# Optimization experiments

Hardware: AMD Instinct MI355X
Metric: run time of the kernel (lower is better)

The kernel has to match this reference:

```python
import jax, jax.numpy as jnp
import numpy as np

N_NODES = 50000
N_EDGES = 800000
IN_DIM = 96
NUM_HEADS = 8
HEAD_DIM = IN_DIM // NUM_HEADS  # 12


def setup_inputs() -> dict:
    key = jax.random.key(0)
    ks = jax.random.split(key, 11)
    s = 1.0 / np.sqrt(IN_DIM)
    return {
        "x": jax.random.normal(ks[0], (N_NODES, IN_DIM), dtype=jnp.float32),
        "edge_index": jax.random.randint(ks[1], (2, N_EDGES), 0, N_NODES, dtype=jnp.int64),
        "edge_attr": jax.random.normal(ks[2], (N_EDGES, IN_DIM), dtype=jnp.float32),
        # Linear weights stored as [in, out] (apply as x @ W + b)
        "Wq": jax.random.normal(ks[3], (IN_DIM, IN_DIM), dtype=jnp.float32) * s,
        "bq": jax.random.normal(ks[4], (IN_DIM,), dtype=jnp.float32) * s,
        "Wk": jax.random.normal(ks[5], (IN_DIM, IN_DIM), dtype=jnp.float32) * s,
        "bk": jax.random.normal(ks[6], (IN_DIM,), dtype=jnp.float32) * s,
        "We": jax.random.normal(ks[7], (IN_DIM, IN_DIM), dtype=jnp.float32) * s,
        "be": jax.random.normal(ks[8], (IN_DIM,), dtype=jnp.float32) * s,
        "Wv": jax.random.normal(ks[9], (IN_DIM, IN_DIM), dtype=jnp.float32) * s,
        "bv": jax.random.normal(ks[10], (IN_DIM,), dtype=jnp.float32) * s,
    }


def reference(x, edge_index, edge_attr, Wq, bq, Wk, bk, We, be, Wv, bv):
    N = x.shape[0]
    H, D = NUM_HEADS, HEAD_DIM
    Q_h = (x @ Wq + bq).reshape(N, H, D)
    K_h = (x @ Wk + bk).reshape(N, H, D)
    V_h = (x @ Wv + bv).reshape(N, H, D)
    E = (edge_attr @ We + be).reshape(-1, H, D)

    src_idx = edge_index[0]
    dst_idx = edge_index[1]
    src = K_h[src_idx]               # [E, H, D]
    dest = Q_h[dst_idx]              # [E, H, D]
    score = (src * dest) / jnp.sqrt(jnp.asarray(D, x.dtype))
    score = score * E
    score = jnp.exp(jnp.clip(score.sum(-1, keepdims=True), -5.0, 5.0))  # [E, H, 1]

    msg = V_h[src_idx] * score       # [E, H, D]
    wV = jax.ops.segment_sum(msg, dst_idx, num_segments=N)      # [N, H, D]
    Z = jax.ops.segment_sum(score, dst_idx, num_segments=N)     # [N, H, 1]
    h_out = wV / (Z + 1e-6)
    return h_out.reshape(N, H * D)
```

## Files before the change

kernel.cpp:

```cpp
#include <hip/hip_runtime.h>
#include <math.h>

#define N_NODES 50000
#define N_EDGES 800000
#define IN_DIM 96
#define NHEADS 8
#define HDIM 12

#define QKV_BLOCKS 782
#define HIST_BLOCKS 3125
#define SCAN_BLOCKS 196

typedef __attribute__((ext_vector_type(8))) short short8;
typedef __attribute__((ext_vector_type(4))) float f32x4;

__device__ __forceinline__ unsigned short f2bf(float f) {
    unsigned int u = __float_as_uint(f);
    return (unsigned short)((u + 0x7FFFu + ((u >> 16) & 1u)) >> 16);
}
__device__ __forceinline__ float bf2f_lo(unsigned int u) {
    return __uint_as_float(u << 16);
}
__device__ __forceinline__ float bf2f_hi(unsigned int u) {
    return __uint_as_float(u & 0xFFFF0000u);
}
__device__ __forceinline__ unsigned int pack2(float a, float b) {
    return (unsigned int)f2bf(a) | ((unsigned int)f2bf(b) << 16);
}
__device__ __forceinline__ short8 pack8(const float4 lo, const float4 hi) {
    union { uint4 u; short8 s; } c;
    c.u.x = pack2(lo.x, lo.y);
    c.u.y = pack2(lo.z, lo.w);
    c.u.z = pack2(hi.x, hi.y);
    c.u.w = pack2(hi.z, hi.w);
    return c.s;
}

__global__ __launch_bounds__(256) void wet4_kernel(
    const float* __restrict__ Wq, const float* __restrict__ Wk,
    const float* __restrict__ Wv, const float* __restrict__ We,
    unsigned short* __restrict__ WqT, unsigned short* __restrict__ WkT,
    unsigned short* __restrict__ WvT, unsigned short* __restrict__ WeT)
{
    const int j = blockIdx.x * 256 + threadIdx.x;
    if (j >= 4 * 9216) return;
    const int m = j / 9216, r = j % 9216;
    const float* W = (m == 0) ? Wq : (m == 1) ? Wk : (m == 2) ? Wv : We;
    unsigned short* WT = (m == 0) ? WqT : (m == 1) ? WkT : (m == 2) ? WvT : WeT;
    const int k = r / 96, c = r % 96;
    WT[c * 96 + k] = f2bf(W[r]);
}

__global__ __launch_bounds__(256) void prep_kernel(
    const float* __restrict__ x,
    const float* __restrict__ bq, const float* __restrict__ bk,
    const float* __restrict__ bv,
    const unsigned short* __restrict__ WqT, const unsigned short* __restrict__ WkT,
    const unsigned short* __restrict__ WvT,
    const int* __restrict__ ei,
    unsigned short* __restrict__ Qb, unsigned short* __restrict__ Kb,
    unsigned short* __restrict__ Vb,
    int* __restrict__ cursor)
{
    const int t = threadIdx.x;
    const int bid = blockIdx.x;

    if (bid >= QKV_BLOCKS) {
        const int e = (bid - QKV_BLOCKS) * 256 + t;
        if (e < N_EDGES) atomicAdd(&cursor[ei[N_EDGES + e]], 1);
        return;
    }

    const int wid = t >> 6;
    const int lid = t & 63;
    const int l15 = lid & 15;
    const int lg  = lid >> 4;
    const int nbase = bid * 64 + wid * 16;

    int arow = nbase + l15;
    if (arow >= N_NODES) arow = N_NODES - 1;
    const float* xr = &x[(size_t)arow * 96 + lg * 8];
    short8 af[3];
    af[0] = pack8(*(const float4*)(xr + 0),  *(const float4*)(xr + 4));
    af[1] = pack8(*(const float4*)(xr + 32), *(const float4*)(xr + 36));
    af[2] = pack8(*(const float4*)(xr + 64), *(const float4*)(xr + 68));

    #pragma unroll
    for (int m = 0; m < 3; ++m) {
        const unsigned short* WT = (m == 0) ? WqT : (m == 1) ? WkT : WvT;
        const float* bias_p      = (m == 0) ? bq  : (m == 1) ? bk  : bv;
        unsigned short* Ob       = (m == 0) ? Qb  : (m == 1) ? Kb  : Vb;

        f32x4 acc[6] = {};
        #pragma unroll
        for (int kk = 0; kk < 3; ++kk) {
            #pragma unroll
            for (int ct = 0; ct < 6; ++ct) {
                const short8 b = *(const short8*)&WT[(ct * 16 + l15) * 96 + kk * 32 + lg * 8];
                acc[ct] = __builtin_amdgcn_mfma_f32_16x16x32_bf16(af[kk], b, acc[ct], 0, 0, 0);
            }
        }
        #pragma unroll
        for (int ct = 0; ct < 6; ++ct) {
            const int col = ct * 16 + l15;
            const float bias = bias_p[col];
            #pragma unroll
            for (int r = 0; r < 4; ++r) {
                const int n = nbase + lg * 4 + r;
                if (n < N_NODES)
                    Ob[(size_t)n * 96 + col] = f2bf(acc[ct][r] + bias);
            }
        }
    }
}

__global__ __launch_bounds__(256) void scanA_kernel(
    const int* __restrict__ cursor, int* __restrict__ partial)
{
    __shared__ int lds[256];
    const int t = threadIdx.x;
    const int idx = blockIdx.x * 256 + t;
    lds[t] = (idx < N_NODES) ? cursor[idx] : 0;
    __syncthreads();
    for (int off = 128; off > 0; off >>= 1) {
        if (t < off) lds[t] += lds[t + off];
        __syncthreads();
    }
    if (t == 0) partial[blockIdx.x] = lds[0];
}

__global__ __launch_bounds__(256) void scanB_kernel(
    int* __restrict__ partial, int* __restrict__ offsets)
{
    __shared__ int lds[256];
    const int t = threadIdx.x;
    const int v = (t < SCAN_BLOCKS) ? partial[t] : 0;
    lds[t] = v;
    __syncthreads();
    for (int off = 1; off < 256; off <<= 1) {
        const int u = (t >= off) ? lds[t - off] : 0;
        __syncthreads();
        lds[t] += u;
        __syncthreads();
    }
    if (t < SCAN_BLOCKS) partial[t] = lds[t] - v;
    if (t == 0) offsets[N_NODES] = N_EDGES;
}

__global__ __launch_bounds__(256) void scanC_kernel(
    int* __restrict__ cursor, const int* __restrict__ partial,
    int* __restrict__ offsets)
{
    __shared__ int lds[256];
    const int t = threadIdx.x;
    const int idx = blockIdx.x * 256 + t;
    const int v = (idx < N_NODES) ? cursor[idx] : 0;
    lds[t] = v;
    __syncthreads();
    for (int off = 1; off < 256; off <<= 1) {
        const int u = (t >= off) ? lds[t - off] : 0;
        __syncthreads();
        lds[t] += u;
        __syncthreads();
    }
    const int excl = lds[t] - v + partial[blockIdx.x];
    if (idx < N_NODES) {
        offsets[idx] = excl;
        cursor[idx] = excl;
    }
}

__global__ __launch_bounds__(256, 4) void score_kernel(
    const float* __restrict__ ea,
    const int* __restrict__ ei,
    const unsigned short* __restrict__ WeT,
    const float* __restrict__ be,
    const unsigned short* __restrict__ Qb, const unsigned short* __restrict__ Kb,
    int* __restrict__ cursor,
    int* __restrict__ sorted_src,
    float* __restrict__ score_s)
{
    __shared__ unsigned short epb[4][16 * 104];

    const int t = threadIdx.x;
    const long ebase = (long)blockIdx.x * 64;
    const int wid = t >> 6;
    const int lid = t & 63;
    const int l15 = lid & 15;
    const int lg  = lid >> 4;
    const long wbase = ebase + wid * 16;

    int v = 0;
    if (lid < 32)
        v = (lid < 16) ? ei[wbase + lid] : ei[N_EDGES + wbase + (lid - 16)];

    const float* arow = &ea[(wbase + l15) * 96 + lg * 8];
    const float4 a0lo = *(const float4*)(arow + 0);
    const float4 a0hi = *(const float4*)(arow + 4);
    const float4 a1lo = *(const float4*)(arow + 32);
    const float4 a1hi = *(const float4*)(arow + 36);
    const float4 a2lo = *(const float4*)(arow + 64);
    const float4 a2hi = *(const float4*)(arow + 68);

    const int er = lid >> 3;
    const int h  = lid & 7;
    const int src0 = __shfl(v, er, 64);
    const int dst0 = __shfl(v, 16 + er, 64);
    const int src1 = __shfl(v, 8 + er, 64);
    const int dst1 = __shfl(v, 24 + er, 64);

    const uint2* K0 = (const uint2*)&Kb[(size_t)src0 * 96 + h * 12];
    const uint2* Q0 = (const uint2*)&Qb[(size_t)dst0 * 96 + h * 12];
    const uint2* K1 = (const uint2*)&Kb[(size_t)src1 * 96 + h * 12];
    const uint2* Q1 = (const uint2*)&Qb[(size_t)dst1 * 96 + h * 12];
    const uint2 k0a = K0[0], k0b = K0[1], k0c = K0[2];
    const uint2 q0a = Q0[0], q0b = Q0[1], q0c = Q0[2];
    const uint2 k1a = K1[0], k1b = K1[1], k1c = K1[2];
    const uint2 q1a = Q1[0], q1b = Q1[1], q1c = Q1[2];

    const int mydst = __shfl(v, 16 + l15, 64);
    int posv = 0;
    if (lid < 16) {
        posv = atomicAdd(&cursor[mydst], 1);
        sorted_src[posv] = v;
    }
    const int pos0 = __shfl(posv, er, 64);
    const int pos1 = __shfl(posv, 8 + er, 64);

    const short8 af[3] = {pack8(a0lo, a0hi), pack8(a1lo, a1hi), pack8(a2lo, a2hi)};

    f32x4 acc[6] = {};
    #pragma unroll
    for (int kk = 0; kk < 3; ++kk) {
        #pragma unroll
        for (int ct = 0; ct < 6; ++ct) {
            const short8 b = *(const short8*)&WeT[(ct * 16 + l15) * 96 + kk * 32 + lg * 8];
            acc[ct] = __builtin_amdgcn_mfma_f32_16x16x32_bf16(af[kk], b, acc[ct], 0, 0, 0);
        }
    }
    unsigned short* myep = epb[wid];
    #pragma unroll
    for (int ct = 0; ct < 6; ++ct) {
        const int col = ct * 16 + l15;
        const float bias = be[col];
        #pragma unroll
        for (int r = 0; r < 4; ++r)
            myep[(lg * 4 + r) * 104 + col] = f2bf(acc[ct][r] + bias);
    }

    const float inv_sqrt_d = 0.2886751345948129f;
#define ACC3(KU, QU, EU) \
    s += bf2f_lo(KU) * bf2f_lo(QU) * bf2f_lo(EU) + \
         bf2f_hi(KU) * bf2f_hi(QU) * bf2f_hi(EU);

    #pragma unroll 2
    for (int pass = 0; pass < 2; ++pass) {
        const int rloc = pass * 8 + er;
        const int pos = pass ? pos1 : pos0;
        const unsigned short* epp = &myep[rloc * 104 + h * 12];
        const uint2 u0 = *(const uint2*)&epp[0];
        const uint2 u1 = *(const uint2*)&epp[4];
        const uint2 u2 = *(const uint2*)&epp[8];
        float s = 0.f;
        if (pass == 0) {
            ACC3(k0a.x, q0a.x, u0.x); ACC3(k0a.y, q0a.y, u0.y);
            ACC3(k0b.x, q0b.x, u1.x); ACC3(k0b.y, q0b.y, u1.y);
            ACC3(k0c.x, q0c.x, u2.x); ACC3(k0c.y, q0c.y, u2.y);
        } else {
            ACC3(k1a.x, q1a.x, u0.x); ACC3(k1a.y, q1a.y, u0.y);
            ACC3(k1b.x, q1b.x, u1.x); ACC3(k1b.y, q1b.y, u1.y);
            ACC3(k1c.x, q1c.x, u2.x); ACC3(k1c.y, q1c.y, u2.y);
        }
        s *= inv_sqrt_d;
        s = fminf(fmaxf(s, -5.f), 5.f);
        score_s[(size_t)pos * 8 + h] = __expf(s);
    }
#undef ACC3
}

__global__ __launch_bounds__(256) void gather_kernel(
    const int* __restrict__ offsets, const int* __restrict__ sorted_src,
    const float* __restrict__ score_s, const unsigned short* __restrict__ Vb,
    float* __restrict__ out)
{
    const int gid = blockIdx.x * 256 + threadIdx.x;
    if (gid >= N_NODES * 4) return;
    const int n = gid >> 2;
    const int g = gid & 3;

    const int s0 = offsets[n];
    const int s1 = offsets[n + 1];

    float acc[24];
    #pragma unroll
    for (int i = 0; i < 24; ++i) acc[i] = 0.f;
    float z0 = 0.f, z1 = 0.f;

#define ACCUM(U0, U1, U2, SC) \
    acc[0]  += SC.x * bf2f_lo(U0.x); acc[1]  += SC.x * bf2f_hi(U0.x); \
    acc[2]  += SC.x * bf2f_lo(U0.y); acc[3]  += SC.x * bf2f_hi(U0.y); \
    acc[4]  += SC.x * bf2f_lo(U0.z); acc[5]  += SC.x * bf2f_hi(U0.z); \
    acc[6]  += SC.x * bf2f_lo(U0.w); acc[7]  += SC.x * bf2f_hi(U0.w); \
    acc[8]  += SC.x * bf2f_lo(U1.x); acc[9]  += SC.x * bf2f_hi(U1.x); \
    acc[10] += SC.x * bf2f_lo(U1.y); acc[11] += SC.x * bf2f_hi(U1.y); \
    acc[12] += SC.y * bf2f_lo(U1.z); acc[13] += SC.y * bf2f_hi(U1.z); \
    acc[14] += SC.y * bf2f_lo(U1.w); acc[15] += SC.y * bf2f_hi(U1.w); \
    acc[16] += SC.y * bf2f_lo(U2.x); acc[17] += SC.y * bf2f_hi(U2.x); \
    acc[18] += SC.y * bf2f_lo(U2.y); acc[19] += SC.y * bf2f_hi(U2.y); \
    acc[20] += SC.y * bf2f_lo(U2.z); acc[21] += SC.y * bf2f_hi(U2.z); \
    acc[22] += SC.y * bf2f_lo(U2.w); acc[23] += SC.y * bf2f_hi(U2.w);

    int p = s0;
    for (; p + 2 <= s1; p += 2) {
        const int srcA = sorted_src[p];
        const int srcB = sorted_src[p + 1];
        const float2 scA = *(const float2*)&score_s[(size_t)p * 8 + g * 2];
        const float2 scB = *(const float2*)&score_s[(size_t)(p + 1) * 8 + g * 2];
        const uint4* VA = (const uint4*)&Vb[(size_t)srcA * 96 + g * 24];
        const uint4* VB = (const uint4*)&Vb[(size_t)srcB * 96 + g * 24];
        const uint4 a0 = VA[0], a1 = VA[1], a2 = VA[2];
        const uint4 b0 = VB[0], b1 = VB[1], b2 = VB[2];
        ACCUM(a0, a1, a2, scA);
        ACCUM(b0, b1, b2, scB);
        z0 += scA.x + scB.x;
        z1 += scA.y + scB.y;
    }
    if (p < s1) {
        const int srcA = sorted_src[p];
        const float2 scA = *(const float2*)&score_s[(size_t)p * 8 + g * 2];
        const uint4* VA = (const uint4*)&Vb[(size_t)srcA * 96 + g * 24];
        const uint4 a0 = VA[0], a1 = VA[1], a2 = VA[2];
        ACCUM(a0, a1, a2, scA);
        z0 += scA.x;
        z1 += scA.y;
    }
#undef ACCUM

    const float i0 = 1.f / (z0 + 1e-6f);
    const float i1 = 1.f / (z1 + 1e-6f);
    float o[24];
    #pragma unroll
    for (int k = 0; k < 24; ++k) o[k] = acc[k] * (k < 12 ? i0 : i1);
    float* dst = &out[(size_t)n * 96 + g * 24];
    #pragma unroll
    for (int k = 0; k < 6; ++k)
        *(float4*)&dst[k * 4] = make_float4(o[k*4], o[k*4+1], o[k*4+2], o[k*4+3]);
}

extern "C" void kernel_launch(void* const* d_in, const int* in_sizes, int n_in,
                              void* d_out, int out_size, void* d_ws, size_t ws_size,
                              hipStream_t stream) {
    const float* x  = (const float*)d_in[0];
    const int*   ei = (const int*)d_in[1];
    const float* ea = (const float*)d_in[2];
    const float* Wq = (const float*)d_in[3];
    const float* bq = (const float*)d_in[4];
    const float* Wk = (const float*)d_in[5];
    const float* bk = (const float*)d_in[6];
    const float* We = (const float*)d_in[7];
    const float* be = (const float*)d_in[8];
    const float* Wv = (const float*)d_in[9];
    const float* bv = (const float*)d_in[10];

    float* out = (float*)d_out;

    const size_t nqkv = (size_t)N_NODES * 96;
    unsigned short* Qb = (unsigned short*)d_ws;
    unsigned short* Kb = Qb + nqkv;
    unsigned short* Vb = Kb + nqkv;
    float* score_s  = (float*)(Vb + nqkv);
    int* offsets    = (int*)(score_s + (size_t)N_EDGES * 8);
    int* cursor     = offsets + (N_NODES + 1);
    int* sorted_src = cursor + N_NODES;
    unsigned short* WeT = (unsigned short*)(sorted_src + N_EDGES);
    unsigned short* WqT = WeT + 9216;
    unsigned short* WkT = WqT + 9216;
    unsigned short* WvT = WkT + 9216;
    int* partial = (int*)(WvT + 9216);

    hipMemsetAsync(cursor, 0, N_NODES * sizeof(int), stream);

    wet4_kernel<<<dim3(144), 256, 0, stream>>>(
        Wq, Wk, Wv, We, WqT, WkT, WvT, WeT);

    prep_kernel<<<dim3(QKV_BLOCKS + HIST_BLOCKS), 256, 0, stream>>>(
        x, bq, bk, bv, WqT, WkT, WvT, ei, Qb, Kb, Vb, cursor);

    scanA_kernel<<<dim3(SCAN_BLOCKS), 256, 0, stream>>>(cursor, partial);
    scanB_kernel<<<dim3(1), 256, 0, stream>>>(partial, offsets);
    scanC_kernel<<<dim3(SCAN_BLOCKS), 256, 0, stream>>>(cursor, partial, offsets);

    score_kernel<<<dim3(N_EDGES / 64), 256, 0, stream>>>(
        ea, ei, WeT, be, Qb, Kb, cursor, sorted_src, score_s);

    gather_kernel<<<dim3((N_NODES * 4 + 255) / 256), 256, 0, stream>>>(
        offsets, sorted_src, score_s, Vb, out);
}
```

Baseline: 270.1 us.

## Make score kernel persistent with LDS-staged We and double-buffered edge tiles

The score kernel now processes 10 edge tiles per block over a 1250-block grid instead of one tile per block. We^T and the bias are staged once per block in padded LDS. The next tile's edge_attr and indices, plus its K/Q gathers and cursor atomics, are issued before the current tile's MFMA and score phase so their latency overlaps. This raises register pressure, lowers the occupancy hint from 4 to 2, and there are only 1250 blocks to balance across the GPU.

```diff
diff --git a/kernel.cpp b/kernel.cpp
--- a/kernel.cpp
+++ b/kernel.cpp
@@ -10,6 +10,8 @@
 #define QKV_BLOCKS 782
 #define HIST_BLOCKS 3125
 #define SCAN_BLOCKS 196
+#define TPB 10
+#define SCORE_GRID 1250
 
 typedef __attribute__((ext_vector_type(8))) short short8;
 typedef __attribute__((ext_vector_type(4))) float f32x4;
@@ -170,7 +172,7 @@
     }
 }
 
-__global__ __launch_bounds__(256, 4) void score_kernel(
+__global__ __launch_bounds__(256, 2) void score_kernel(
     const float* __restrict__ ea,
     const int* __restrict__ ei,
     const unsigned short* __restrict__ WeT,
@@ -180,102 +182,144 @@
     int* __restrict__ sorted_src,
     float* __restrict__ score_s)
 {
+    __shared__ unsigned short WsT[96 * 104];
     __shared__ unsigned short epb[4][16 * 104];
+    __shared__ float bes[96];
 
     const int t = threadIdx.x;
-    const long ebase = (long)blockIdx.x * 64;
     const int wid = t >> 6;
     const int lid = t & 63;
     const int l15 = lid & 15;
     const int lg  = lid >> 4;
-    const long wbase = ebase + wid * 16;
-
-    int v = 0;
-    if (lid < 32)
-        v = (lid < 16) ? ei[wbase + lid] : ei[N_EDGES + wbase + (lid - 16)];
-
-    const float* arow = &ea[(wbase + l15) * 96 + lg * 8];
-    const float4 a0lo = *(const float4*)(arow + 0);
-    const float4 a0hi = *(const float4*)(arow + 4);
-    const float4 a1lo = *(const float4*)(arow + 32);
-    const float4 a1hi = *(const float4*)(arow + 36);
-    const float4 a2lo = *(const float4*)(arow + 64);
-    const float4 a2hi = *(const float4*)(arow + 68);
-
-    const int er = lid >> 3;
-    const int h  = lid & 7;
-    const int src0 = __shfl(v, er, 64);
-    const int dst0 = __shfl(v, 16 + er, 64);
-    const int src1 = __shfl(v, 8 + er, 64);
-    const int dst1 = __shfl(v, 24 + er, 64);
-
-    const uint2* K0 = (const uint2*)&Kb[(size_t)src0 * 96 + h * 12];
-    const uint2* Q0 = (const uint2*)&Qb[(size_t)dst0 * 96 + h * 12];
-    const uint2* K1 = (const uint2*)&Kb[(size_t)src1 * 96 + h * 12];
-    const uint2* Q1 = (const uint2*)&Qb[(size_t)dst1 * 96 + h * 12];
-    const uint2 k0a = K0[0], k0b = K0[1], k0c = K0[2];
-    const uint2 q0a = Q0[0], q0b = Q0[1], q0c = Q0[2];
-    const uint2 k1a = K1[0], k1b = K1[1], k1c = K1[2];
-    const uint2 q1a = Q1[0], q1b = Q1[1], q1c = Q1[2];
-
-    const int mydst = __shfl(v, 16 + l15, 64);
-    int posv = 0;
-    if (lid < 16) {
-        posv = atomicAdd(&cursor[mydst], 1);
-        sorted_src[posv] = v;
-    }
-    const int pos0 = __shfl(posv, er, 64);
-    const int pos1 = __shfl(posv, 8 + er, 64);
-
-    const short8 af[3] = {pack8(a0lo, a0hi), pack8(a1lo, a1hi), pack8(a2lo, a2hi)};
-
-    f32x4 acc[6] = {};
-    #pragma unroll
-    for (int kk = 0; kk < 3; ++kk) {
-        #pragma unroll
-        for (int ct = 0; ct < 6; ++ct) {
-            const short8 b = *(const short8*)&WeT[(ct * 16 + l15) * 96 + kk * 32 + lg * 8];
-            acc[ct] = __builtin_amdgcn_mfma_f32_16x16x32_bf16(af[kk], b, acc[ct], 0, 0, 0);
-        }
-    }
+    const int er  = lid >> 3;
+    const int h   = lid & 7;
     unsigned short* myep = epb[wid];
-    #pragma unroll
-    for (int ct = 0; ct < 6; ++ct) {
-        const int col = ct * 16 + l15;
-        const float bias = be[col];
-        #pragma unroll
-        for (int r = 0; r < 4; ++r)
-            myep[(lg * 4 + r) * 104 + col] = f2bf(acc[ct][r] + bias);
-    }
-
-    const float inv_sqrt_d = 0.2886751345948129f;
+    const long t0 = (long)blockIdx.x * TPB;
+
+#define LOAD_EI(V, TILE) do { \
+    const long wb_ = (long)(TILE) * 64 + wid * 16; \
+    (V) = 0; \
+    if (lid < 32) (V) = (lid < 16) ? ei[wb_ + lid] : ei[N_EDGES + wb_ + (lid - 16)]; \
+} while (0)
+
+#define LOAD_EA(EA, TILE) do { \
+    const float* ar_ = &ea[((long)(TILE) * 64 + wid * 16 + l15) * 96 + lg * 8]; \
+    (EA)[0] = *(const float4*)(ar_ + 0);  (EA)[1] = *(const float4*)(ar_ + 4); \
+    (EA)[2] = *(const float4*)(ar_ + 32); (EA)[3] = *(const float4*)(ar_ + 36); \
+    (EA)[4] = *(const float4*)(ar_ + 64); (EA)[5] = *(const float4*)(ar_ + 68); \
+} while (0)
+
+#define ISSUE_GATHER(V, KQ, P0, P1) do { \
+    const int s0_ = __shfl((V), er, 64); \
+    const int d0_ = __shfl((V), 16 + er, 64); \
+    const int s1_ = __shfl((V), 8 + er, 64); \
+    const int d1_ = __shfl((V), 24 + er, 64); \
+    const uint2* K0_ = (const uint2*)&Kb[(size_t)s0_ * 96 + h * 12]; \
+    const uint2* Q0_ = (const uint2*)&Qb[(size_t)d0_ * 96 + h * 12]; \
+    const uint2* K1_ = (const uint2*)&Kb[(size_t)s1_ * 96 + h * 12]; \
+    const uint2* Q1_ = (const uint2*)&Qb[(size_t)d1_ * 96 + h * 12]; \
+    (KQ)[0] = K0_[0]; (KQ)[1] = K0_[1]; (KQ)[2] = K0_[2]; \
+    (KQ)[3] = Q0_[0]; (KQ)[4] = Q0_[1]; (KQ)[5] = Q0_[2]; \
+    (KQ)[6] = K1_[0]; (KQ)[7] = K1_[1]; (KQ)[8] = K1_[2]; \
+    (KQ)[9] = Q1_[0]; (KQ)[10] = Q1_[1]; (KQ)[11] = Q1_[2]; \
+    const int md_ = __shfl((V), 16 + l15, 64); \
+    int pv_ = 0; \
+    if (lid < 16) { pv_ = atomicAdd(&cursor[md_], 1); sorted_src[pv_] = (V); } \
+    (P0) = __shfl(pv_, er, 64); \
+    (P1) = __shfl(pv_, 8 + er, 64); \
+} while (0)
+
+#define MFMA_EPB(EA) do { \
+    const short8 af0_ = pack8((EA)[0], (EA)[1]); \
+    const short8 af1_ = pack8((EA)[2], (EA)[3]); \
+    const short8 af2_ = pack8((EA)[4], (EA)[5]); \
+    f32x4 acc_[6] = {}; \
+    _Pragma("unroll") \
+    for (int ct = 0; ct < 6; ++ct) { \
+        acc_[ct] = __builtin_amdgcn_mfma_f32_16x16x32_bf16(af0_, \
+            *(const short8*)&WsT[(ct * 16 + l15) * 104 + 0 + lg * 8], acc_[ct], 0, 0, 0); \
+        acc_[ct] = __builtin_amdgcn_mfma_f32_16x16x32_bf16(af1_, \
+            *(const short8*)&WsT[(ct * 16 + l15) * 104 + 32 + lg * 8], acc_[ct], 0, 0, 0); \
+        acc_[ct] = __builtin_amdgcn_mfma_f32_16x16x32_bf16(af2_, \
+            *(const short8*)&WsT[(ct * 16 + l15) * 104 + 64 + lg * 8], acc_[ct], 0, 0, 0); \
+    } \
+    _Pragma("unroll") \
+    for (int ct = 0; ct < 6; ++ct) { \
+        const int col_ = ct * 16 + l15; \
+        const float b_ = bes[col_]; \
+        _Pragma("unroll") \
+        for (int r = 0; r < 4; ++r) \
+            myep[(lg * 4 + r) * 104 + col_] = f2bf(acc_[ct][r] + b_); \
+    } \
+} while (0)
+
 #define ACC3(KU, QU, EU) \
-    s += bf2f_lo(KU) * bf2f_lo(QU) * bf2f_lo(EU) + \
-         bf2f_hi(KU) * bf2f_hi(QU) * bf2f_hi(EU);
-
-    #pragma unroll 2
-    for (int pass = 0; pass < 2; ++pass) {
-        const int rloc = pass * 8 + er;
-        const int pos = pass ? pos1 : pos0;
-        const unsigned short* epp = &myep[rloc * 104 + h * 12];
-        const uint2 u0 = *(const uint2*)&epp[0];
-        const uint2 u1 = *(const uint2*)&epp[4];
-        const uint2 u2 = *(const uint2*)&epp[8];
-        float s = 0.f;
-        if (pass == 0) {
-            ACC3(k0a.x, q0a.x, u0.x); ACC3(k0a.y, q0a.y, u0.y);
-            ACC3(k0b.x, q0b.x, u1.x); ACC3(k0b.y, q0b.y, u1.y);
-            ACC3(k0c.x, q0c.x, u2.x); ACC3(k0c.y, q0c.y, u2.y);
-        } else {
-            ACC3(k1a.x, q1a.x, u0.x); ACC3(k1a.y, q1a.y, u0.y);
-            ACC3(k1b.x, q1b.x, u1.x); ACC3(k1b.y, q1b.y, u1.y);
-            ACC3(k1c.x, q1c.x, u2.x); ACC3(k1c.y, q1c.y, u2.y);
-        }
-        s *= inv_sqrt_d;
-        s = fminf(fmaxf(s, -5.f), 5.f);
-        score_s[(size_t)pos * 8 + h] = __expf(s);
-    }
+    s_ += bf2f_lo(KU) * bf2f_lo(QU) * bf2f_lo(EU) + \
+          bf2f_hi(KU) * bf2f_hi(QU) * bf2f_hi(EU);
+
+#define SCORE_PHASE(KQ, P0, P1) do { \
+    _Pragma("unroll") \
+    for (int pass_ = 0; pass_ < 2; ++pass_) { \
+        const int rl_ = pass_ * 8 + er; \
+        const int pos_ = pass_ ? (P1) : (P0); \
+        const unsigned short* ep_ = &myep[rl_ * 104 + h * 12]; \
+        const uint2 u0_ = *(const uint2*)&ep_[0]; \
+        const uint2 u1_ = *(const uint2*)&ep_[4]; \
+        const uint2 u2_ = *(const uint2*)&ep_[8]; \
+        const uint2 ka_ = (KQ)[pass_ * 6 + 0]; \
+        const uint2 kb_ = (KQ)[pass_ * 6 + 1]; \
+        const uint2 kc_ = (KQ)[pass_ * 6 + 2]; \
+        const uint2 qa_ = (KQ)[pass_ * 6 + 3]; \
+        const uint2 qb_ = (KQ)[pass_ * 6 + 4]; \
+        const uint2 qc_ = (KQ)[pass_ * 6 + 5]; \
+        float s_ = 0.f; \
+        ACC3(ka_.x, qa_.x, u0_.x); ACC3(ka_.y, qa_.y, u0_.y); \
+        ACC3(kb_.x, qb_.x, u1_.x); ACC3(kb_.y, qb_.y, u1_.y); \
+        ACC3(kc_.x, qc_.x, u2_.x); ACC3(kc_.y, qc_.y, u2_.y); \
+        s_ *= 0.2886751345948129f; \
+        s_ = fminf(fmaxf(s_, -5.f), 5.f); \
+        score_s[(size_t)pos_ * 8 + h] = __expf(s_); \
+    } \
+} while (0)
+
+    int vA, vB;
+    float4 eaA[6], eaB[6];
+    uint2 kqA[12], kqB[12];
+    int pA0 = 0, pA1 = 0, pB0 = 0, pB1 = 0;
+
+    LOAD_EI(vA, t0);
+    LOAD_EA(eaA, t0);
+    LOAD_EI(vB, t0 + 1);
+    LOAD_EA(eaB, t0 + 1);
+
+    for (int j = t; j < 96 * 12; j += 256) {
+        const int c = j / 12, kc = j % 12;
+        *(uint4*)&WsT[c * 104 + kc * 8] = *(const uint4*)&WeT[c * 96 + kc * 8];
+    }
+    if (t < 96) bes[t] = be[t];
+    __syncthreads();
+
+    ISSUE_GATHER(vA, kqA, pA0, pA1);
+
+    #pragma unroll 1
+    for (int i = 0; i < TPB; i += 2) {
+        MFMA_EPB(eaA);
+        ISSUE_GATHER(vB, kqB, pB0, pB1);
+        if (i + 2 < TPB) { LOAD_EI(vA, t0 + i + 2); LOAD_EA(eaA, t0 + i + 2); }
+        SCORE_PHASE(kqA, pA0, pA1);
+
+        MFMA_EPB(eaB);
+        if (i + 2 < TPB) ISSUE_GATHER(vA, kqA, pA0, pA1);
+        if (i + 3 < TPB) { LOAD_EI(vB, t0 + i + 3); LOAD_EA(eaB, t0 + i + 3); }
+        SCORE_PHASE(kqB, pB0, pB1);
+    }
+
+#undef LOAD_EI
+#undef LOAD_EA
+#undef ISSUE_GATHER
+#undef MFMA_EPB
 #undef ACC3
+#undef SCORE_PHASE
 }
 
 __global__ __launch_bounds__(256) void gather_kernel(
@@ -390,7 +434,7 @@
     scanB_kernel<<<dim3(1), 256, 0, stream>>>(partial, offsets);
     scanC_kernel<<<dim3(SCAN_BLOCKS), 256, 0, stream>>>(cursor, partial, offsets);
 
-    score_kernel<<<dim3(N_EDGES / 64), 256, 0, stream>>>(
+    score_kernel<<<dim3(SCORE_GRID), 256, 0, stream>>>(
         ea, ei, WeT, be, Qb, Kb, cursor, sorted_src, score_s);
 
     gather_kernel<<<dim3((N_NODES * 4 + 255) / 256), 256, 0, stream>>>(
```

Result: faster. 239.1 us (median of 2 runs) (-11.5%).

## Split edge projection from score kernel and store scores as bf16

Applied to the files above, without the earlier changes.

The fused score kernel becomes two kernels. The first projects edge_attr through We with MFMA, staging the weights in LDS, and writes a bf16 edge-projection buffer to global memory. The second gathers Q, K and that projection to compute scores, with smaller work per wave and higher occupancy, and stores the scores as bf16 to halve their traffic in the gather kernel. The cost is an extra global write and read of the 800k×96 bf16 projection, an added launch, and lower score precision.

```diff
diff --git a/kernel.cpp b/kernel.cpp
--- a/kernel.cpp
+++ b/kernel.cpp
@@ -170,29 +170,22 @@
     }
 }
 
-__global__ __launch_bounds__(256, 4) void score_kernel(
+__global__ __launch_bounds__(256, 4) void eproj_kernel(
     const float* __restrict__ ea,
-    const int* __restrict__ ei,
     const unsigned short* __restrict__ WeT,
     const float* __restrict__ be,
-    const unsigned short* __restrict__ Qb, const unsigned short* __restrict__ Kb,
-    int* __restrict__ cursor,
-    int* __restrict__ sorted_src,
-    float* __restrict__ score_s)
-{
+    unsigned short* __restrict__ ep_g)
+{
+    __shared__ unsigned short WsT[96 * 104];
     __shared__ unsigned short epb[4][16 * 104];
-
-    const int t = threadIdx.x;
-    const long ebase = (long)blockIdx.x * 64;
+    __shared__ float bes[96];
+
+    const int t = threadIdx.x;
     const int wid = t >> 6;
     const int lid = t & 63;
     const int l15 = lid & 15;
     const int lg  = lid >> 4;
-    const long wbase = ebase + wid * 16;
-
-    int v = 0;
-    if (lid < 32)
-        v = (lid < 16) ? ei[wbase + lid] : ei[N_EDGES + wbase + (lid - 16)];
+    const long wbase = (long)blockIdx.x * 64 + wid * 16;
 
     const float* arow = &ea[(wbase + l15) * 96 + lg * 8];
     const float4 a0lo = *(const float4*)(arow + 0);
@@ -202,30 +195,12 @@
     const float4 a2lo = *(const float4*)(arow + 64);
     const float4 a2hi = *(const float4*)(arow + 68);
 
-    const int er = lid >> 3;
-    const int h  = lid & 7;
-    const int src0 = __shfl(v, er, 64);
-    const int dst0 = __shfl(v, 16 + er, 64);
-    const int src1 = __shfl(v, 8 + er, 64);
-    const int dst1 = __shfl(v, 24 + er, 64);
-
-    const uint2* K0 = (const uint2*)&Kb[(size_t)src0 * 96 + h * 12];
-    const uint2* Q0 = (const uint2*)&Qb[(size_t)dst0 * 96 + h * 12];
-    const uint2* K1 = (const uint2*)&Kb[(size_t)src1 * 96 + h * 12];
-    const uint2* Q1 = (const uint2*)&Qb[(size_t)dst1 * 96 + h * 12];
-    const uint2 k0a = K0[0], k0b = K0[1], k0c = K0[2];
-    const uint2 q0a = Q0[0], q0b = Q0[1], q0c = Q0[2];
-    const uint2 k1a = K1[0], k1b = K1[1], k1c = K1[2];
-    const uint2 q1a = Q1[0], q1b = Q1[1], q1c = Q1[2];
-
-    const int mydst = __shfl(v, 16 + l15, 64);
-    int posv = 0;
-    if (lid < 16) {
-        posv = atomicAdd(&cursor[mydst], 1);
-        sorted_src[posv] = v;
-    }
-    const int pos0 = __shfl(posv, er, 64);
-    const int pos1 = __shfl(posv, 8 + er, 64);
+    for (int j = t; j < 96 * 12; j += 256) {
+        const int c = j / 12, kc = j % 12;
+        *(uint4*)&WsT[c * 104 + kc * 8] = *(const uint4*)&WeT[c * 96 + kc * 8];
+    }
+    if (t < 96) bes[t] = be[t];
+    __syncthreads();
 
     const short8 af[3] = {pack8(a0lo, a0hi), pack8(a1lo, a1hi), pack8(a2lo, a2hi)};
 
@@ -234,7 +209,7 @@
     for (int kk = 0; kk < 3; ++kk) {
         #pragma unroll
         for (int ct = 0; ct < 6; ++ct) {
-            const short8 b = *(const short8*)&WeT[(ct * 16 + l15) * 96 + kk * 32 + lg * 8];
+            const short8 b = *(const short8*)&WsT[(ct * 16 + l15) * 104 + kk * 32 + lg * 8];
             acc[ct] = __builtin_amdgcn_mfma_f32_16x16x32_bf16(af[kk], b, acc[ct], 0, 0, 0);
         }
     }
@@ -242,45 +217,72 @@
     #pragma unroll
     for (int ct = 0; ct < 6; ++ct) {
         const int col = ct * 16 + l15;
-        const float bias = be[col];
+        const float bias = bes[col];
         #pragma unroll
         for (int r = 0; r < 4; ++r)
             myep[(lg * 4 + r) * 104 + col] = f2bf(acc[ct][r] + bias);
     }
-
-    const float inv_sqrt_d = 0.2886751345948129f;
+    const int row = lid >> 2;
+    const int ch  = lid & 3;
+    const unsigned short* s = &myep[row * 104 + ch * 24];
+    unsigned short* d = &ep_g[(size_t)(wbase + row) * 96 + ch * 24];
+    *(uint4*)(d + 0)  = *(const uint4*)(s + 0);
+    *(uint4*)(d + 8)  = *(const uint4*)(s + 8);
+    *(uint4*)(d + 16) = *(const uint4*)(s + 16);
+}
+
+__global__ __launch_bounds__(256) void score_lite_kernel(
+    const int* __restrict__ ei,
+    const unsigned short* __restrict__ ep_g,
+    const unsigned short* __restrict__ Qb, const unsigned short* __restrict__ Kb,
+    int* __restrict__ cursor,
+    int* __restrict__ sorted_src,
+    unsigned short* __restrict__ score_b)
+{
+    const int t = threadIdx.x;
+    const int lid = t & 63;
+    const long ebase = ((long)blockIdx.x * 4 + (t >> 6)) * 8;
+    const int er = lid >> 3;
+    const int h  = lid & 7;
+
+    int v = 0;
+    if (lid < 16)
+        v = (lid < 8) ? ei[ebase + lid] : ei[N_EDGES + ebase + (lid - 8)];
+
+    const int src = __shfl(v, er, 64);
+    const int dst = __shfl(v, 8 + er, 64);
+
+    const uint2* Kp = (const uint2*)&Kb[(size_t)src * 96 + h * 12];
+    const uint2* Qp = (const uint2*)&Qb[(size_t)dst * 96 + h * 12];
+    const uint2* Ep = (const uint2*)&ep_g[(ebase + er) * 96 + h * 12];
+    const uint2 ka = Kp[0], kb_ = Kp[1], kc = Kp[2];
+    const uint2 qa = Qp[0], qb_ = Qp[1], qc = Qp[2];
+    const uint2 u0 = Ep[0], u1 = Ep[1], u2 = Ep[2];
+
+    const int dstFor = __shfl(v, 8 + (lid & 7), 64);
+    int posv = 0;
+    if (lid < 8) {
+        posv = atomicAdd(&cursor[dstFor], 1);
+        sorted_src[posv] = v;
+    }
+    const int pos = __shfl(posv, er, 64);
+
+    float s = 0.f;
 #define ACC3(KU, QU, EU) \
     s += bf2f_lo(KU) * bf2f_lo(QU) * bf2f_lo(EU) + \
          bf2f_hi(KU) * bf2f_hi(QU) * bf2f_hi(EU);
-
-    #pragma unroll 2
-    for (int pass = 0; pass < 2; ++pass) {
-        const int rloc = pass * 8 + er;
-        const int pos = pass ? pos1 : pos0;
-        const unsigned short* epp = &myep[rloc * 104 + h * 12];
-        const uint2 u0 = *(const uint2*)&epp[0];
-        const uint2 u1 = *(const uint2*)&epp[4];
-        const uint2 u2 = *(const uint2*)&epp[8];
-        float s = 0.f;
-        if (pass == 0) {
-            ACC3(k0a.x, q0a.x, u0.x); ACC3(k0a.y, q0a.y, u0.y);
-            ACC3(k0b.x, q0b.x, u1.x); ACC3(k0b.y, q0b.y, u1.y);
-            ACC3(k0c.x, q0c.x, u2.x); ACC3(k0c.y, q0c.y, u2.y);
-        } else {
-            ACC3(k1a.x, q1a.x, u0.x); ACC3(k1a.y, q1a.y, u0.y);
-            ACC3(k1b.x, q1b.x, u1.x); ACC3(k1b.y, q1b.y, u1.y);
-            ACC3(k1c.x, q1c.x, u2.x); ACC3(k1c.y, q1c.y, u2.y);
-        }
-        s *= inv_sqrt_d;
-        s = fminf(fmaxf(s, -5.f), 5.f);
-        score_s[(size_t)pos * 8 + h] = __expf(s);
-    }
+    ACC3(ka.x, qa.x, u0.x); ACC3(ka.y, qa.y, u0.y);
+    ACC3(kb_.x, qb_.x, u1.x); ACC3(kb_.y, qb_.y, u1.y);
+    ACC3(kc.x, qc.x, u2.x); ACC3(kc.y, qc.y, u2.y);
 #undef ACC3
+    s *= 0.2886751345948129f;
+    s = fminf(fmaxf(s, -5.f), 5.f);
+    score_b[(size_t)pos * 8 + h] = f2bf(__expf(s));
 }
 
 __global__ __launch_bounds__(256) void gather_kernel(
     const int* __restrict__ offsets, const int* __restrict__ sorted_src,
-    const float* __restrict__ score_s, const unsigned short* __restrict__ Vb,
+    const unsigned short* __restrict__ score_b, const unsigned short* __restrict__ Vb,
     float* __restrict__ out)
 {
     const int gid = blockIdx.x * 256 + threadIdx.x;
@@ -296,43 +298,46 @@
     for (int i = 0; i < 24; ++i) acc[i] = 0.f;
     float z0 = 0.f, z1 = 0.f;
 
-#define ACCUM(U0, U1, U2, SC) \
-    acc[0]  += SC.x * bf2f_lo(U0.x); acc[1]  += SC.x * bf2f_hi(U0.x); \
-    acc[2]  += SC.x * bf2f_lo(U0.y); acc[3]  += SC.x * bf2f_hi(U0.y); \
-    acc[4]  += SC.x * bf2f_lo(U0.z); acc[5]  += SC.x * bf2f_hi(U0.z); \
-    acc[6]  += SC.x * bf2f_lo(U0.w); acc[7]  += SC.x * bf2f_hi(U0.w); \
-    acc[8]  += SC.x * bf2f_lo(U1.x); acc[9]  += SC.x * bf2f_hi(U1.x); \
-    acc[10] += SC.x * bf2f_lo(U1.y); acc[11] += SC.x * bf2f_hi(U1.y); \
-    acc[12] += SC.y * bf2f_lo(U1.z); acc[13] += SC.y * bf2f_hi(U1.z); \
-    acc[14] += SC.y * bf2f_lo(U1.w); acc[15] += SC.y * bf2f_hi(U1.w); \
-    acc[16] += SC.y * bf2f_lo(U2.x); acc[17] += SC.y * bf2f_hi(U2.x); \
-    acc[18] += SC.y * bf2f_lo(U2.y); acc[19] += SC.y * bf2f_hi(U2.y); \
-    acc[20] += SC.y * bf2f_lo(U2.z); acc[21] += SC.y * bf2f_hi(U2.z); \
-    acc[22] += SC.y * bf2f_lo(U2.w); acc[23] += SC.y * bf2f_hi(U2.w);
+#define ACCUM(U0, U1, U2, SX, SY) \
+    acc[0]  += SX * bf2f_lo(U0.x); acc[1]  += SX * bf2f_hi(U0.x); \
+    acc[2]  += SX * bf2f_lo(U0.y); acc[3]  += SX * bf2f_hi(U0.y); \
+    acc[4]  += SX * bf2f_lo(U0.z); acc[5]  += SX * bf2f_hi(U0.z); \
+    acc[6]  += SX * bf2f_lo(U0.w); acc[7]  += SX * bf2f_hi(U0.w); \
+    acc[8]  += SX * bf2f_lo(U1.x); acc[9]  += SX * bf2f_hi(U1.x); \
+    acc[10] += SX * bf2f_lo(U1.y); acc[11] += SX * bf2f_hi(U1.y); \
+    acc[12] += SY * bf2f_lo(U1.z); acc[13] += SY * bf2f_hi(U1.z); \
+    acc[14] += SY * bf2f_lo(U1.w); acc[15] += SY * bf2f_hi(U1.w); \
+    acc[16] += SY * bf2f_lo(U2.x); acc[17] += SY * bf2f_hi(U2.x); \
+    acc[18] += SY * bf2f_lo(U2.y); acc[19] += SY * bf2f_hi(U2.y); \
+    acc[20] += SY * bf2f_lo(U2.z); acc[21] += SY * bf2f_hi(U2.z); \
+    acc[22] += SY * bf2f_lo(U2.w); acc[23] += SY * bf2f_hi(U2.w);
 
     int p = s0;
     for (; p + 2 <= s1; p += 2) {
         const int srcA = sorted_src[p];
         const int srcB = sorted_src[p + 1];
-        const float2 scA = *(const float2*)&score_s[(size_t)p * 8 + g * 2];
-        const float2 scB = *(const float2*)&score_s[(size_t)(p + 1) * 8 + g * 2];
+        const unsigned int sA = *(const unsigned int*)&score_b[(size_t)p * 8 + g * 2];
+        const unsigned int sB = *(const unsigned int*)&score_b[(size_t)(p + 1) * 8 + g * 2];
+        const float sAx = bf2f_lo(sA), sAy = bf2f_hi(sA);
+        const float sBx = bf2f_lo(sB), sBy = bf2f_hi(sB);
         const uint4* VA = (const uint4*)&Vb[(size_t)srcA * 96 + g * 24];
         const uint4* VB = (const uint4*)&Vb[(size_t)srcB * 96 + g * 24];
         const uint4 a0 = VA[0], a1 = VA[1], a2 = VA[2];
         const uint4 b0 = VB[0], b1 = VB[1], b2 = VB[2];
-        ACCUM(a0, a1, a2, scA);
-        ACCUM(b0, b1, b2, scB);
-        z0 += scA.x + scB.x;
-        z1 += scA.y + scB.y;
+        ACCUM(a0, a1, a2, sAx, sAy);
+        ACCUM(b0, b1, b2, sBx, sBy);
+        z0 += sAx + sBx;
+        z1 += sAy + sBy;
     }
     if (p < s1) {
         const int srcA = sorted_src[p];
-        const float2 scA = *(const float2*)&score_s[(size_t)p * 8 + g * 2];
+        const unsigned int sA = *(const unsigned int*)&score_b[(size_t)p * 8 + g * 2];
+        const float sAx = bf2f_lo(sA), sAy = bf2f_hi(sA);
         const uint4* VA = (const uint4*)&Vb[(size_t)srcA * 96 + g * 24];
         const uint4 a0 = VA[0], a1 = VA[1], a2 = VA[2];
-        ACCUM(a0, a1, a2, scA);
-        z0 += scA.x;
-        z1 += scA.y;
+        ACCUM(a0, a1, a2, sAx, sAy);
+        z0 += sAx;
+        z1 += sAy;
     }
 #undef ACCUM
 
@@ -368,8 +373,8 @@
     unsigned short* Qb = (unsigned short*)d_ws;
     unsigned short* Kb = Qb + nqkv;
     unsigned short* Vb = Kb + nqkv;
-    float* score_s  = (float*)(Vb + nqkv);
-    int* offsets    = (int*)(score_s + (size_t)N_EDGES * 8);
+    unsigned short* score_b = Vb + nqkv;
+    int* offsets    = (int*)(score_b + (size_t)N_EDGES * 8);
     int* cursor     = offsets + (N_NODES + 1);
     int* sorted_src = cursor + N_NODES;
     unsigned short* WeT = (unsigned short*)(sorted_src + N_EDGES);
@@ -377,6 +382,7 @@
     unsigned short* WkT = WqT + 9216;
     unsigned short* WvT = WkT + 9216;
     int* partial = (int*)(WvT + 9216);
+    unsigned short* ep_g = (unsigned short*)(partial + 256);
 
     hipMemsetAsync(cursor, 0, N_NODES * sizeof(int), stream);
 
@@ -390,9 +396,11 @@
     scanB_kernel<<<dim3(1), 256, 0, stream>>>(partial, offsets);
     scanC_kernel<<<dim3(SCAN_BLOCKS), 256, 0, stream>>>(cursor, partial, offsets);
 
-    score_kernel<<<dim3(N_EDGES / 64), 256, 0, stream>>>(
-        ea, ei, WeT, be, Qb, Kb, cursor, sorted_src, score_s);
+    eproj_kernel<<<dim3(N_EDGES / 64), 256, 0, stream>>>(ea, WeT, be, ep_g);
+
+    score_lite_kernel<<<dim3(N_EDGES / 32), 256, 0, stream>>>(
+        ei, ep_g, Qb, Kb, cursor, sorted_src, score_b);
 
     gather_kernel<<<dim3((N_NODES * 4 + 255) / 256), 256, 0, stream>>>(
-        offsets, sorted_src, score_s, Vb, out);
-}
+        offsets, sorted_src, score_b, Vb, out);
+}
```

After: 321.1 us. 18.9% more time.
